# Kernel optimization log

Measured on AMD Instinct MI355X. Metric: run time of the kernel, lower is better.

## Reference

```python
import jax, jax.numpy as jnp
import numpy as np
from math import sqrt

BS, SEQ, NV, DM, K = 16, 1024, 512, 256, 8
EPS = 0.05  # sinkhorn epsilon
TEMP = 0.07  # concrete-bernoulli temperature


def setup_inputs() -> dict:
    key = jax.random.key(0)
    k1, k2, k3 = jax.random.split(key, 3)
    x = jax.random.normal(k1, (BS, SEQ, NV), jnp.float32)
    # nn.Linear(seq_len, d_model): weight [d_model, seq_len], bias [d_model]
    W = jax.random.normal(k2, (DM, SEQ), jnp.float32) / sqrt(SEQ)
    b = jnp.zeros((DM,), jnp.float32)
    cluster_emb = jax.random.normal(k3, (K, DM), jnp.float32) / sqrt(DM)
    return {"x": x, "W": W, "b": b, "cluster_emb": cluster_emb}


def _l2norm(z):
    # F.normalize(x, dim=1, p=2) with eps=1e-12 clamp
    n = jnp.maximum(jnp.linalg.norm(z, axis=1, keepdims=True), 1e-12)
    return z / n


def _sinkhorn(q):
    Q = jnp.exp(q / EPS)
    return Q / jnp.sum(Q, axis=1, keepdims=True)


def _concrete_bern(p, key):
    u = jax.random.uniform(key, p.shape, p.dtype, 1e-10, 1.0 - 1e-10)
    noise = jnp.log(u) - jnp.log1p(-u)
    logit = jnp.log(p + 1e-10) - jnp.log(1.0 - p + 1e-10)
    return jax.nn.sigmoid((logit + noise) / TEMP)


def _forward(x, W, b, cluster_emb):
    bs, S, nv = x.shape
    d = W.shape[0]
    k = cluster_emb.shape[0]
    # permute -> [bs, nv, S], Linear(S -> d)
    x_emb = jnp.einsum('bsv,ds->bvd', x, W) + b  # [bs, nv, d]
    x_flat = x_emb.reshape(-1, d)  # [bs*nv, d]
    # cosine-similarity cluster logits
    prob = (_l2norm(x_flat) @ _l2norm(cluster_emb).T).reshape(bs, nv, k)
    prob_temp = _sinkhorn(prob.reshape(-1, k)).reshape(bs, nv, k)  # individual probs
    prob_avg = _sinkhorn(jnp.mean(prob, axis=0))  # [nv, k]
    mask = _concrete_bern(prob_avg, jax.random.key(42))  # [nv, k]
    # CrossAttention with n_heads=1 (dropout inactive in eval)
    scale = 1.0 / sqrt(d)
    scores = jnp.einsum('kd,bvd->bkv', cluster_emb, x_emb)  # [bs, k, nv]
    A = jax.nn.softmax(scale * scores, axis=-1) * mask.T[None]  # masked attn
    V = jnp.einsum('bkv,bvd->bkd', A, x_emb)  # [bs, k, d]
    cluster_emb_avg = jnp.mean(V, axis=0)  # [k, d] (stored attribute in torch)
    # cluster_base_encoding: straight-through bernoulli, broadcast over seq_len
    soft = prob_temp.transpose(2, 0, 1)[..., None]  # [k, bs, nv, 1]
    u = jax.random.uniform(jax.random.key(7), soft.shape, soft.dtype)
    bern = (u < jax.lax.stop_gradient(soft)).astype(soft.dtype)
    extend = jnp.broadcast_to(bern, (k, bs, nv, S))  # [k, bs, nv, S]
    hard = soft + jax.lax.stop_gradient(extend - soft)  # straight-through
    return hard


def reference(x, W, b, cluster_emb):
    return _forward(x, W, b, cluster_emb)
```

## Files before the change

### kernel.cpp

```cpp
#include <hip/hip_runtime.h>
#include <math.h>
#include <stdint.h>

#define BS 16
#define SEQ 1024
#define NV 512
#define DM 256
#define NK 8

typedef __attribute__((ext_vector_type(8))) short bf16x8;
typedef __attribute__((ext_vector_type(4))) float f32x4;

__device__ double g_WC[NK * SEQ];
__device__ double g_Bk[NK];
__device__ __align__(16) unsigned short g_x0[BS * NV * SEQ];
__device__ __align__(16) unsigned short g_x1[BS * NV * SEQ];
__device__ __align__(16) unsigned short g_x2[BS * NV * SEQ];
__device__ __align__(16) unsigned short g_w0[DM * SEQ];
__device__ __align__(16) unsigned short g_w1[DM * SEQ];
__device__ __align__(16) unsigned short g_w2[DM * SEQ];
__device__ __align__(16) float g_zp[4 * BS * NV * DM];
__device__ double g_nn2[BS * NV];
__device__ double g_Dp[8 * BS * NV * NK];
__device__ unsigned char g_bits[BS * NV];

__device__ __forceinline__ void threefry2x32_key7(uint32_t x0, uint32_t x1,
                                                  uint32_t& o0, uint32_t& o1) {
    const uint32_t k0 = 0u, k1 = 7u;
    const uint32_t k2 = k0 ^ k1 ^ 0x1BD11BDAu;
    uint32_t v0 = x0 + k0, v1 = x1 + k1;
#define TF_ROUND(r) { v0 += v1; v1 = (v1 << (r)) | (v1 >> (32 - (r))); v1 ^= v0; }
    TF_ROUND(13) TF_ROUND(15) TF_ROUND(26) TF_ROUND(6)
    v0 += k1; v1 += k2 + 1u;
    TF_ROUND(17) TF_ROUND(29) TF_ROUND(16) TF_ROUND(24)
    v0 += k2; v1 += k0 + 2u;
    TF_ROUND(13) TF_ROUND(15) TF_ROUND(26) TF_ROUND(6)
    v0 += k0; v1 += k1 + 3u;
    TF_ROUND(17) TF_ROUND(29) TF_ROUND(16) TF_ROUND(24)
    v0 += k1; v1 += k2 + 4u;
    TF_ROUND(13) TF_ROUND(15) TF_ROUND(26) TF_ROUND(6)
    v0 += k2; v1 += k0 + 5u;
#undef TF_ROUND
    o0 = v0; o1 = v1;
}

__device__ __forceinline__ float bits_to_uniform(uint32_t b) {
    return __uint_as_float((b >> 9) | 0x3F800000u) - 1.0f;
}

__device__ __forceinline__ unsigned short f2bf(float f) {
    uint32_t u = __float_as_uint(f);
    return (unsigned short)((u + 0x7FFFu + ((u >> 16) & 1u)) >> 16);
}
__device__ __forceinline__ float bf2f(unsigned short h) {
    return __uint_as_float(((uint32_t)h) << 16);
}
__device__ __forceinline__ void split3(float f, unsigned short& h0,
                                       unsigned short& h1, unsigned short& h2) {
    h0 = f2bf(f);
    float r1 = f - bf2f(h0);
    h1 = f2bf(r1);
    float r2 = r1 - bf2f(h1);
    h2 = f2bf(r2);
}

__device__ __forceinline__ void cp16s(const unsigned short* g, unsigned short* l) {
    __builtin_amdgcn_global_load_lds(
        (const __attribute__((address_space(1))) void*)g,
        (__attribute__((address_space(3))) void*)l,
        16, 0, 0);
}

__global__ __launch_bounds__(256) void prep_kernel(
        const float* __restrict__ W, const float* __restrict__ bias,
        const float* __restrict__ ce) {
    __shared__ double red[256];
    __shared__ double cen[256];
    const int t = threadIdx.x;
    const int bid = blockIdx.x;

    if (bid >= 32) {
        const int base = (bid - 32) * 4096 + t * 16;
        uint32_t p0[8], p1[8], p2[8];
#pragma unroll
        for (int i = 0; i < 16; ++i) {
            unsigned short h0, h1, h2;
            split3(W[base + i], h0, h1, h2);
            if (i & 1) {
                p0[i >> 1] |= (uint32_t)h0 << 16;
                p1[i >> 1] |= (uint32_t)h1 << 16;
                p2[i >> 1] |= (uint32_t)h2 << 16;
            } else {
                p0[i >> 1] = h0; p1[i >> 1] = h1; p2[i >> 1] = h2;
            }
        }
        *(uint4*)&g_w0[base]     = make_uint4(p0[0], p0[1], p0[2], p0[3]);
        *(uint4*)&g_w0[base + 8] = make_uint4(p0[4], p0[5], p0[6], p0[7]);
        *(uint4*)&g_w1[base]     = make_uint4(p1[0], p1[1], p1[2], p1[3]);
        *(uint4*)&g_w1[base + 8] = make_uint4(p1[4], p1[5], p1[6], p1[7]);
        *(uint4*)&g_w2[base]     = make_uint4(p2[0], p2[1], p2[2], p2[3]);
        *(uint4*)&g_w2[base + 8] = make_uint4(p2[4], p2[5], p2[6], p2[7]);
        return;
    }

    const int k = bid >> 2;
    const int schunk = bid & 3;

    double c = (double)ce[k * DM + t];
    red[t] = c * c;
    __syncthreads();
    for (int off = 128; off > 0; off >>= 1) {
        if (t < off) red[t] += red[t + off];
        __syncthreads();
    }
    double nc = fmax(sqrt(red[0]), 1e-12);
    cen[t] = c / nc;
    __syncthreads();
    red[t] = (double)bias[t] * cen[t];
    __syncthreads();
    for (int off = 128; off > 0; off >>= 1) {
        if (t < off) red[t] += red[t + off];
        __syncthreads();
    }
    if (t == 0 && schunk == 0) g_Bk[k] = red[0];

    const int s = schunk * 256 + t;
    double acc = 0.0;
#pragma unroll 8
    for (int d = 0; d < DM; ++d)
        acc += cen[d] * (double)W[(size_t)d * SEQ + s];
    g_WC[(size_t)k * SEQ + s] = acc;
}

__global__ __launch_bounds__(256) void xsplit_kernel(const float* __restrict__ x) {
    __shared__ float tile[64][65];
    const int t = threadIdx.x;
    const int stile = blockIdx.x >> 3, vtile = blockIdx.x & 7;
    const int b = blockIdx.y;
    const int s0 = stile * 64, v0 = vtile * 64;
    const float* xb = x + ((size_t)b * SEQ + s0) * NV + v0;

#pragma unroll
    for (int p = 0; p < 16; ++p) {
        int lin = p * 256 + t;
        int sl = lin >> 6, vv = lin & 63;
        tile[sl][vv] = xb[(size_t)sl * NV + vv];
    }
    __syncthreads();

    const int vr = t >> 2, g = t & 3;
    const size_t obase = ((size_t)b * NV + v0 + vr) * SEQ + s0 + g * 16;
    uint32_t p0[8], p1[8], p2[8];
#pragma unroll
    for (int i = 0; i < 16; ++i) {
        unsigned short h0, h1, h2;
        split3(tile[g * 16 + i][vr], h0, h1, h2);
        if (i & 1) {
            p0[i >> 1] |= (uint32_t)h0 << 16;
            p1[i >> 1] |= (uint32_t)h1 << 16;
            p2[i >> 1] |= (uint32_t)h2 << 16;
        } else {
            p0[i >> 1] = h0; p1[i >> 1] = h1; p2[i >> 1] = h2;
        }
    }
    *(uint4*)&g_x0[obase]     = make_uint4(p0[0], p0[1], p0[2], p0[3]);
    *(uint4*)&g_x0[obase + 8] = make_uint4(p0[4], p0[5], p0[6], p0[7]);
    *(uint4*)&g_x1[obase]     = make_uint4(p1[0], p1[1], p1[2], p1[3]);
    *(uint4*)&g_x1[obase + 8] = make_uint4(p1[4], p1[5], p1[6], p1[7]);
    *(uint4*)&g_x2[obase]     = make_uint4(p2[0], p2[1], p2[2], p2[3]);
    *(uint4*)&g_x2[obase + 8] = make_uint4(p2[4], p2[5], p2[6], p2[7]);
}

__global__ __launch_bounds__(256) void gemm_kernel() {
    __shared__ __align__(16) unsigned short xs3[3][64 * 32];
    __shared__ __align__(16) unsigned short ws3[3][128 * 32];

    const int t = threadIdx.x;
    const int kblk = blockIdx.x & 3;
    const int dblk = blockIdx.x >> 2;
    const int vblk = blockIdx.y;
    const int b    = blockIdx.z;
    const int v0 = vblk * 64, d0 = dblk * 128;
    const int w = t >> 6, l = t & 63;

    const int srow = l >> 2;
    const int sk8  = ((l & 3) ^ ((l >> 2) & 3)) * 8;
    const int rrow = l & 15;
    const int rsl  = ((l >> 4) ^ (l & 3)) * 8;

    const size_t xbase = ((size_t)b * NV + v0) * SEQ;
    const size_t wbase = (size_t)d0 * SEQ;
    const unsigned short* xsrc[3] = {g_x0 + xbase, g_x1 + xbase, g_x2 + xbase};
    const unsigned short* wsrc[3] = {g_w0 + wbase, g_w1 + wbase, g_w2 + wbase};

    f32x4 acc[4][2];
#pragma unroll
    for (int mb = 0; mb < 4; ++mb)
#pragma unroll
        for (int nb = 0; nb < 2; ++nb) acc[mb][nb] = (f32x4){0.f, 0.f, 0.f, 0.f};

    for (int c = 0; c < 8; ++c) {
        const int s0 = kblk * 256 + c * 32;
        __syncthreads();
#pragma unroll
        for (int sp = 0; sp < 3; ++sp) {
            cp16s(&xsrc[sp][(size_t)(w * 16 + srow) * SEQ + s0 + sk8],
                  &xs3[sp][w * 16 * 32]);
            cp16s(&wsrc[sp][(size_t)(w * 32 + srow) * SEQ + s0 + sk8],
                  &ws3[sp][w * 32 * 32]);
            cp16s(&wsrc[sp][(size_t)(w * 32 + 16 + srow) * SEQ + s0 + sk8],
                  &ws3[sp][(w * 32 + 16) * 32]);
        }
        __syncthreads();

        bf16x8 a[3][4], bb[3][2];
#pragma unroll
        for (int sp = 0; sp < 3; ++sp) {
#pragma unroll
            for (int mb = 0; mb < 4; ++mb)
                a[sp][mb] = *(const bf16x8*)&xs3[sp][(mb * 16 + rrow) * 32 + rsl];
#pragma unroll
            for (int nb = 0; nb < 2; ++nb)
                bb[sp][nb] = *(const bf16x8*)
                    &ws3[sp][(w * 32 + nb * 16 + rrow) * 32 + rsl];
        }
#pragma unroll
        for (int mb = 0; mb < 4; ++mb)
#pragma unroll
            for (int nb = 0; nb < 2; ++nb) {
                f32x4 v = acc[mb][nb];
                v = __builtin_amdgcn_mfma_f32_16x16x32_bf16(a[1][mb], bb[1][nb], v, 0, 0, 0);
                v = __builtin_amdgcn_mfma_f32_16x16x32_bf16(a[0][mb], bb[2][nb], v, 0, 0, 0);
                v = __builtin_amdgcn_mfma_f32_16x16x32_bf16(a[2][mb], bb[0][nb], v, 0, 0, 0);
                v = __builtin_amdgcn_mfma_f32_16x16x32_bf16(a[0][mb], bb[1][nb], v, 0, 0, 0);
                v = __builtin_amdgcn_mfma_f32_16x16x32_bf16(a[1][mb], bb[0][nb], v, 0, 0, 0);
                v = __builtin_amdgcn_mfma_f32_16x16x32_bf16(a[0][mb], bb[0][nb], v, 0, 0, 0);
                acc[mb][nb] = v;
            }
    }

    const int rowb = (l >> 4) * 4;
#pragma unroll
    for (int mb = 0; mb < 4; ++mb)
#pragma unroll
        for (int nb = 0; nb < 2; ++nb) {
            const int d = d0 + w * 32 + nb * 16 + (l & 15);
#pragma unroll
            for (int r = 0; r < 4; ++r) {
                const int v = v0 + mb * 16 + rowb + r;
                g_zp[(size_t)kblk * (BS * NV * DM) +
                     ((size_t)b * NV + v) * DM + d] = acc[mb][nb][r];
            }
        }
}

__global__ __launch_bounds__(256) void cd_kernel(
        const float* __restrict__ bias, const float* __restrict__ x) {
    __shared__ double sm[3072];
    const int t = threadIdx.x;
    const int bid = blockIdx.x;

    if (bid < 512) {
        const int vg = bid >> 4;
        const int b  = bid & 15;
        const int vl = t >> 4, dg = t & 15;
        const int v = vg * 16 + vl;

        const size_t bvbase = ((size_t)b * NV + v) * DM + dg * 16;
        double sq = 0.0;
#pragma unroll
        for (int m = 0; m < 16; m += 4) {
            float4 p0 = *(const float4*)&g_zp[(size_t)0 * (BS * NV * DM) + bvbase + m];
            float4 p1 = *(const float4*)&g_zp[(size_t)1 * (BS * NV * DM) + bvbase + m];
            float4 p2 = *(const float4*)&g_zp[(size_t)2 * (BS * NV * DM) + bvbase + m];
            float4 p3 = *(const float4*)&g_zp[(size_t)3 * (BS * NV * DM) + bvbase + m];
            float4 bb = *(const float4*)&bias[dg * 16 + m];
            double z0 = (double)p0.x + (double)p1.x + (double)p2.x + (double)p3.x + (double)bb.x;
            double z1 = (double)p0.y + (double)p1.y + (double)p2.y + (double)p3.y + (double)bb.y;
            double z2 = (double)p0.z + (double)p1.z + (double)p2.z + (double)p3.z + (double)bb.z;
            double z3 = (double)p0.w + (double)p1.w + (double)p2.w + (double)p3.w + (double)bb.w;
            sq += z0 * z0 + z1 * z1 + z2 * z2 + z3 * z3;
        }
        sm[vl * 17 + dg] = sq;
        __syncthreads();
        if (dg == 0) {
            double s = 0.0;
#pragma unroll
            for (int i = 0; i < 16; ++i) s += sm[vl * 17 + i];
            g_nn2[b * NV + v] = s;
        }
        return;
    }

    const int did  = bid - 512;
    const int vblk = did & 7;
    const int b    = (did >> 3) & 15;
    const int sc   = did >> 7;
    const int v0 = vblk * 64;
    const int ss = sc * 128;

    double* wcd = sm;
    double* dw  = sm + 1024;

#pragma unroll
    for (int j = 0; j < 4; ++j) {
        int idx = j * 256 + t;
        wcd[idx] = g_WC[(size_t)(idx >> 7) * SEQ + ss + (idx & 127)];
    }
    __syncthreads();

    const int vl = t & 63, w = t >> 6;
    const float* xp = x + (size_t)b * SEQ * NV + v0 + vl;
    double D[NK];
#pragma unroll
    for (int k = 0; k < NK; ++k) D[k] = 0.0;
    const int sw = w * 32;
    for (int i = 0; i < 32; ++i) {
        int sl = sw + i;
        double xv = (double)xp[(size_t)(ss + sl) * NV];
#pragma unroll
        for (int k = 0; k < NK; ++k) D[k] += xv * wcd[k * 128 + sl];
    }
#pragma unroll
    for (int k = 0; k < NK; ++k) dw[(w * 64 + vl) * NK + k] = D[k];
    __syncthreads();

    const int v = t & 63, k2 = (t >> 6) * 2;
#pragma unroll
    for (int j = 0; j < 2; ++j) {
        int k = k2 + j;
        double s = dw[(0 * 64 + v) * NK + k] + dw[(1 * 64 + v) * NK + k] +
                   dw[(2 * 64 + v) * NK + k] + dw[(3 * 64 + v) * NK + k];
        g_Dp[(((size_t)sc * BS + b) * NV + v0 + v) * NK + k] = s;
    }
}

__global__ __launch_bounds__(256) void finalize_kernel() {
    const int bv = blockIdx.x * 256 + threadIdx.x;
    double n = fmax(sqrt(g_nn2[bv]), 1e-12);

    double D[NK];
#pragma unroll
    for (int k = 0; k < NK; ++k) D[k] = g_Bk[k];
#pragma unroll
    for (int sc = 0; sc < 8; ++sc) {
#pragma unroll
        for (int k = 0; k < NK; ++k)
            D[k] += g_Dp[((size_t)sc * (BS * NV) + bv) * NK + k];
    }

    double p[NK], sum = 0.0;
#pragma unroll
    for (int k = 0; k < NK; ++k) {
        p[k] = exp((D[k] / n) / 0.05);
        sum += p[k];
    }
    unsigned int byte = 0;
#pragma unroll
    for (int k = 0; k < NK; ++k) {
        uint32_t i = (uint32_t)(k * (BS * NV) + bv);
        uint32_t y0, y1;
        threefry2x32_key7(0u, i, y0, y1);
        float u = bits_to_uniform(y0 ^ y1);
        if ((double)u < p[k] / sum) byte |= 1u << k;
    }
    g_bits[bv] = (unsigned char)byte;
}

__global__ __launch_bounds__(256) void write_kernel(float* __restrict__ out) {
    const int t = threadIdx.x;
    const size_t r0 = (size_t)blockIdx.x * 8;
#pragma unroll
    for (int j = 0; j < 8; ++j) {
        size_t r = r0 + j;
        unsigned int bv = (unsigned int)(r & 8191u);
        unsigned int k  = (unsigned int)(r >> 13);
        float v = ((g_bits[bv] >> k) & 1u) ? 1.0f : 0.0f;
        float4 val = make_float4(v, v, v, v);
        ((float4*)(out + r * 1024))[t] = val;
    }
}

extern "C" void kernel_launch(void* const* d_in, const int* in_sizes, int n_in,
                              void* d_out, int out_size, void* d_ws, size_t ws_size,
                              hipStream_t stream) {
    const float* x    = (const float*)d_in[0];
    const float* W    = (const float*)d_in[1];
    const float* bias = (const float*)d_in[2];
    const float* ce   = (const float*)d_in[3];
    float* out = (float*)d_out;

    prep_kernel<<<dim3(96), dim3(256), 0, stream>>>(W, bias, ce);
    xsplit_kernel<<<dim3(128, 16), dim3(256), 0, stream>>>(x);
    gemm_kernel<<<dim3(8, 8, 16), dim3(256), 0, stream>>>();
    cd_kernel<<<dim3(1536), dim3(256), 0, stream>>>(bias, x);
    finalize_kernel<<<dim3(32), dim3(256), 0, stream>>>();
    write_kernel<<<dim3(8192), dim3(256), 0, stream>>>(out);
}
```

Measured before the change: 392.6 us.

## Fuse norm reduction into GEMM epilogue, drop split-K partials, double-buffer tiles

```diff
diff --git a/kernel.cpp b/kernel.cpp
--- a/kernel.cpp
+++ b/kernel.cpp
@@ -19,8 +19,7 @@
 __device__ __align__(16) unsigned short g_w0[DM * SEQ];
 __device__ __align__(16) unsigned short g_w1[DM * SEQ];
 __device__ __align__(16) unsigned short g_w2[DM * SEQ];
-__device__ __align__(16) float g_zp[4 * BS * NV * DM];
-__device__ double g_nn2[BS * NV];
+__device__ double g_nn2p[2][BS * NV];
 __device__ double g_Dp[8 * BS * NV * NK];
 __device__ unsigned char g_bits[BS * NV];
 
@@ -171,16 +170,18 @@
     *(uint4*)&g_x2[obase + 8] = make_uint4(p2[4], p2[5], p2[6], p2[7]);
 }
 
-__global__ __launch_bounds__(256) void gemm_kernel() {
-    __shared__ __align__(16) unsigned short xs3[3][64 * 32];
-    __shared__ __align__(16) unsigned short ws3[3][128 * 32];
+#define KC 32
+
+__global__ __launch_bounds__(256) void gemm_kernel(const float* __restrict__ bias) {
+    __shared__ __align__(16) unsigned short xs[2][3][32 * 32];
+    __shared__ __align__(16) unsigned short ws[2][3][128 * 32];
+    __shared__ double dred[4][32];
 
     const int t = threadIdx.x;
-    const int kblk = blockIdx.x & 3;
-    const int dblk = blockIdx.x >> 2;
-    const int vblk = blockIdx.y;
+    const int dblk = blockIdx.x;
+    const int vt   = blockIdx.y;
     const int b    = blockIdx.z;
-    const int v0 = vblk * 64, d0 = dblk * 128;
+    const int v0 = vt * 32, d0 = dblk * 128;
     const int w = t >> 6, l = t & 63;
 
     const int srow = l >> 2;
@@ -193,39 +194,54 @@
     const unsigned short* xsrc[3] = {g_x0 + xbase, g_x1 + xbase, g_x2 + xbase};
     const unsigned short* wsrc[3] = {g_w0 + wbase, g_w1 + wbase, g_w2 + wbase};
 
-    f32x4 acc[4][2];
-#pragma unroll
-    for (int mb = 0; mb < 4; ++mb)
-#pragma unroll
-        for (int nb = 0; nb < 2; ++nb) acc[mb][nb] = (f32x4){0.f, 0.f, 0.f, 0.f};
-
-    for (int c = 0; c < 8; ++c) {
-        const int s0 = kblk * 256 + c * 32;
-        __syncthreads();
+    f32x4 acc[2][2];
+    double zac[2][2][4];
+#pragma unroll
+    for (int mb = 0; mb < 2; ++mb)
+#pragma unroll
+        for (int nb = 0; nb < 2; ++nb) {
+            acc[mb][nb] = (f32x4){0.f, 0.f, 0.f, 0.f};
+#pragma unroll
+            for (int r = 0; r < 4; ++r) zac[mb][nb][r] = 0.0;
+        }
+
+#define STAGE(BUF, C)                                                          \
+    {                                                                          \
+        const int S0 = (C) * KC;                                               \
+        _Pragma("unroll")                                                      \
+        for (int sp = 0; sp < 3; ++sp) {                                       \
+            cp16s(&wsrc[sp][(size_t)(w * 32 + srow) * SEQ + S0 + sk8],         \
+                  &ws[BUF][sp][(w * 32) * 32]);                                \
+            cp16s(&wsrc[sp][(size_t)(w * 32 + 16 + srow) * SEQ + S0 + sk8],    \
+                  &ws[BUF][sp][(w * 32 + 16) * 32]);                           \
+        }                                                                      \
+        if (w < 3) {                                                           \
+            cp16s(&xsrc[w][(size_t)srow * SEQ + S0 + sk8], &xs[BUF][w][0]);    \
+            cp16s(&xsrc[w][(size_t)(16 + srow) * SEQ + S0 + sk8],              \
+                  &xs[BUF][w][16 * 32]);                                       \
+        }                                                                      \
+    }
+
+    STAGE(0, 0)
+    __syncthreads();
+
+    for (int c = 0; c < 32; ++c) {
+        const int buf = c & 1;
+        if (c < 31) STAGE(buf ^ 1, c + 1)
+
+        bf16x8 a[3][2], bb[3][2];
 #pragma unroll
         for (int sp = 0; sp < 3; ++sp) {
-            cp16s(&xsrc[sp][(size_t)(w * 16 + srow) * SEQ + s0 + sk8],
-                  &xs3[sp][w * 16 * 32]);
-            cp16s(&wsrc[sp][(size_t)(w * 32 + srow) * SEQ + s0 + sk8],
-                  &ws3[sp][w * 32 * 32]);
-            cp16s(&wsrc[sp][(size_t)(w * 32 + 16 + srow) * SEQ + s0 + sk8],
-                  &ws3[sp][(w * 32 + 16) * 32]);
-        }
-        __syncthreads();
-
-        bf16x8 a[3][4], bb[3][2];
-#pragma unroll
-        for (int sp = 0; sp < 3; ++sp) {
-#pragma unroll
-            for (int mb = 0; mb < 4; ++mb)
-                a[sp][mb] = *(const bf16x8*)&xs3[sp][(mb * 16 + rrow) * 32 + rsl];
+#pragma unroll
+            for (int mb = 0; mb < 2; ++mb)
+                a[sp][mb] = *(const bf16x8*)&xs[buf][sp][(mb * 16 + rrow) * 32 + rsl];
 #pragma unroll
             for (int nb = 0; nb < 2; ++nb)
                 bb[sp][nb] = *(const bf16x8*)
-                    &ws3[sp][(w * 32 + nb * 16 + rrow) * 32 + rsl];
-        }
-#pragma unroll
-        for (int mb = 0; mb < 4; ++mb)
+                    &ws[buf][sp][(w * 32 + nb * 16 + rrow) * 32 + rsl];
+        }
+#pragma unroll
+        for (int mb = 0; mb < 2; ++mb)
 #pragma unroll
             for (int nb = 0; nb < 2; ++nb) {
                 f32x4 v = acc[mb][nb];
@@ -237,75 +253,79 @@
                 v = __builtin_amdgcn_mfma_f32_16x16x32_bf16(a[0][mb], bb[0][nb], v, 0, 0, 0);
                 acc[mb][nb] = v;
             }
-    }
-
-    const int rowb = (l >> 4) * 4;
-#pragma unroll
-    for (int mb = 0; mb < 4; ++mb)
+
+        if ((c & 7) == 7) {
+#pragma unroll
+            for (int mb = 0; mb < 2; ++mb)
+#pragma unroll
+                for (int nb = 0; nb < 2; ++nb) {
+#pragma unroll
+                    for (int r = 0; r < 4; ++r)
+                        zac[mb][nb][r] += (double)acc[mb][nb][r];
+                    acc[mb][nb] = (f32x4){0.f, 0.f, 0.f, 0.f};
+                }
+        }
+
+        __syncthreads();
+    }
+#undef STAGE
+
+    double sv[2][4];
+#pragma unroll
+    for (int mb = 0; mb < 2; ++mb)
+#pragma unroll
+        for (int r = 0; r < 4; ++r) sv[mb][r] = 0.0;
+#pragma unroll
+    for (int mb = 0; mb < 2; ++mb)
 #pragma unroll
         for (int nb = 0; nb < 2; ++nb) {
             const int d = d0 + w * 32 + nb * 16 + (l & 15);
+            const double bd = (double)bias[d];
 #pragma unroll
             for (int r = 0; r < 4; ++r) {
-                const int v = v0 + mb * 16 + rowb + r;
-                g_zp[(size_t)kblk * (BS * NV * DM) +
-                     ((size_t)b * NV + v) * DM + d] = acc[mb][nb][r];
+                double z = zac[mb][nb][r] + bd;
+                sv[mb][r] += z * z;
             }
         }
-}
-
-__global__ __launch_bounds__(256) void cd_kernel(
-        const float* __restrict__ bias, const float* __restrict__ x) {
-    __shared__ double sm[3072];
+#pragma unroll
+    for (int mb = 0; mb < 2; ++mb)
+#pragma unroll
+        for (int r = 0; r < 4; ++r) {
+            double s = sv[mb][r];
+            s += __shfl_xor(s, 1);
+            s += __shfl_xor(s, 2);
+            s += __shfl_xor(s, 4);
+            s += __shfl_xor(s, 8);
+            sv[mb][r] = s;
+        }
+    if ((l & 15) == 0) {
+#pragma unroll
+        for (int mb = 0; mb < 2; ++mb)
+#pragma unroll
+            for (int r = 0; r < 4; ++r)
+                dred[w][mb * 16 + (l >> 4) * 4 + r] = sv[mb][r];
+    }
+    __syncthreads();
+    if (t < 32) {
+        double s = dred[0][t] + dred[1][t] + dred[2][t] + dred[3][t];
+        g_nn2p[dblk][b * NV + v0 + t] = s;
+    }
+}
+
+__global__ __launch_bounds__(256) void dkern(const float* __restrict__ x) {
+    __shared__ double wcd[NK][128];
+    __shared__ double dw[4][64][NK];
     const int t = threadIdx.x;
-    const int bid = blockIdx.x;
-
-    if (bid < 512) {
-        const int vg = bid >> 4;
-        const int b  = bid & 15;
-        const int vl = t >> 4, dg = t & 15;
-        const int v = vg * 16 + vl;
-
-        const size_t bvbase = ((size_t)b * NV + v) * DM + dg * 16;
-        double sq = 0.0;
-#pragma unroll
-        for (int m = 0; m < 16; m += 4) {
-            float4 p0 = *(const float4*)&g_zp[(size_t)0 * (BS * NV * DM) + bvbase + m];
-            float4 p1 = *(const float4*)&g_zp[(size_t)1 * (BS * NV * DM) + bvbase + m];
-            float4 p2 = *(const float4*)&g_zp[(size_t)2 * (BS * NV * DM) + bvbase + m];
-            float4 p3 = *(const float4*)&g_zp[(size_t)3 * (BS * NV * DM) + bvbase + m];
-            float4 bb = *(const float4*)&bias[dg * 16 + m];
-            double z0 = (double)p0.x + (double)p1.x + (double)p2.x + (double)p3.x + (double)bb.x;
-            double z1 = (double)p0.y + (double)p1.y + (double)p2.y + (double)p3.y + (double)bb.y;
-            double z2 = (double)p0.z + (double)p1.z + (double)p2.z + (double)p3.z + (double)bb.z;
-            double z3 = (double)p0.w + (double)p1.w + (double)p2.w + (double)p3.w + (double)bb.w;
-            sq += z0 * z0 + z1 * z1 + z2 * z2 + z3 * z3;
-        }
-        sm[vl * 17 + dg] = sq;
-        __syncthreads();
-        if (dg == 0) {
-            double s = 0.0;
-#pragma unroll
-            for (int i = 0; i < 16; ++i) s += sm[vl * 17 + i];
-            g_nn2[b * NV + v] = s;
-        }
-        return;
-    }
-
-    const int did  = bid - 512;
-    const int vblk = did & 7;
-    const int b    = (did >> 3) & 15;
-    const int sc   = did >> 7;
+    const int vblk = blockIdx.x;
+    const int b    = blockIdx.y;
+    const int sc   = blockIdx.z;
     const int v0 = vblk * 64;
     const int ss = sc * 128;
 
-    double* wcd = sm;
-    double* dw  = sm + 1024;
-
 #pragma unroll
     for (int j = 0; j < 4; ++j) {
         int idx = j * 256 + t;
-        wcd[idx] = g_WC[(size_t)(idx >> 7) * SEQ + ss + (idx & 127)];
+        ((double*)wcd)[idx] = g_WC[(size_t)(idx >> 7) * SEQ + ss + (idx & 127)];
     }
     __syncthreads();
 
@@ -319,25 +339,24 @@
         int sl = sw + i;
         double xv = (double)xp[(size_t)(ss + sl) * NV];
 #pragma unroll
-        for (int k = 0; k < NK; ++k) D[k] += xv * wcd[k * 128 + sl];
-    }
-#pragma unroll
-    for (int k = 0; k < NK; ++k) dw[(w * 64 + vl) * NK + k] = D[k];
+        for (int k = 0; k < NK; ++k) D[k] += xv * wcd[k][sl];
+    }
+#pragma unroll
+    for (int k = 0; k < NK; ++k) dw[w][vl][k] = D[k];
     __syncthreads();
 
     const int v = t & 63, k2 = (t >> 6) * 2;
 #pragma unroll
     for (int j = 0; j < 2; ++j) {
         int k = k2 + j;
-        double s = dw[(0 * 64 + v) * NK + k] + dw[(1 * 64 + v) * NK + k] +
-                   dw[(2 * 64 + v) * NK + k] + dw[(3 * 64 + v) * NK + k];
+        double s = dw[0][v][k] + dw[1][v][k] + dw[2][v][k] + dw[3][v][k];
         g_Dp[(((size_t)sc * BS + b) * NV + v0 + v) * NK + k] = s;
     }
 }
 
 __global__ __launch_bounds__(256) void finalize_kernel() {
     const int bv = blockIdx.x * 256 + threadIdx.x;
-    double n = fmax(sqrt(g_nn2[bv]), 1e-12);
+    double n = fmax(sqrt(g_nn2p[0][bv] + g_nn2p[1][bv]), 1e-12);
 
     double D[NK];
 #pragma unroll
@@ -392,8 +411,8 @@
 
     prep_kernel<<<dim3(96), dim3(256), 0, stream>>>(W, bias, ce);
     xsplit_kernel<<<dim3(128, 16), dim3(256), 0, stream>>>(x);
-    gemm_kernel<<<dim3(8, 8, 16), dim3(256), 0, stream>>>();
-    cd_kernel<<<dim3(1536), dim3(256), 0, stream>>>(bias, x);
+    gemm_kernel<<<dim3(2, 16, 16), dim3(256), 0, stream>>>(bias);
+    dkern<<<dim3(8, 16, 8), dim3(256), 0, stream>>>(x);
     finalize_kernel<<<dim3(32), dim3(256), 0, stream>>>();
     write_kernel<<<dim3(8192), dim3(256), 0, stream>>>(out);
 }
```

Result: no change. 396.4 us (+1.0%).
